# Optimization experiments

Measured on AMD Instinct MI355X. Metric: run time of the kernel, lower is better.

The kernel has to match this reference:

```python
import jax, jax.numpy as jnp
import numpy as np

B, T, D, HD = 4, 4096, 1024, 64

def setup_inputs() -> dict:
    key = jax.random.key(0)
    kx, kq, kk, kv = jax.random.split(key, 4)
    s = 1.0 / np.sqrt(D)
    return {
        "x": jax.random.normal(kx, (B, T, D), dtype=jnp.float32),
        "wq": jax.random.uniform(kq, (HD, D), jnp.float32, -s, s),
        "wk": jax.random.uniform(kk, (HD, D), jnp.float32, -s, s),
        "wv": jax.random.uniform(kv, (HD, D), jnp.float32, -s, s),
    }

def reference(x, wq, wk, wv):
    # Linear(D, headDim, bias=False): y = x @ W.T with W of shape [headDim, D]
    Q = jnp.einsum('btD,dD->btd', x, wq)
    K = jnp.einsum('bsD,dD->bsd', x, wk)
    V = jnp.einsum('bsD,dD->bsd', x, wv)
    head_dim = wq.shape[0]
    logits = jnp.einsum('btd,bsd->bts', Q, K) / jnp.sqrt(jnp.float32(head_dim))
    attn = jax.nn.softmax(logits, axis=-1)
    return jnp.einsum('bts,bsd->btd', attn, V)
```

## Files before the change

kernel.cpp:

```cpp
#include <hip/hip_runtime.h>
#include <math.h>

#define TLEN 4096
#define BD   1024
#define HDIM 64
#define NB   4

typedef __attribute__((ext_vector_type(8))) short bf16x8;
typedef __attribute__((ext_vector_type(4))) float f32x4;

typedef const __attribute__((address_space(1))) unsigned char* gp_t;
typedef __attribute__((address_space(3))) unsigned char* lp_t;

__device__ __forceinline__ void async_cp16(const void* g, void* l) {
    __builtin_amdgcn_global_load_lds((gp_t)g, (lp_t)l, 16, 0, 0);
}

__device__ __forceinline__ unsigned short f2bf(float f) {
    union { float f; unsigned u; } v; v.f = f;
    unsigned r = v.u + 0x7FFF + ((v.u >> 16) & 1);
    return (unsigned short)(r >> 16);
}

__device__ __forceinline__ bf16x8 cvt8(const float4 a, const float4 b) {
    bf16x8 r;
    r[0] = (short)f2bf(a.x); r[1] = (short)f2bf(a.y);
    r[2] = (short)f2bf(a.z); r[3] = (short)f2bf(a.w);
    r[4] = (short)f2bf(b.x); r[5] = (short)f2bf(b.y);
    r[6] = (short)f2bf(b.z); r[7] = (short)f2bf(b.w);
    return r;
}

__global__ __launch_bounds__(256) void wconv_kernel(
    const float* __restrict__ wq, const float* __restrict__ wk,
    const float* __restrict__ wv, unsigned short* __restrict__ wbf)
{
    const int r = blockIdx.x;
    const float* src = (r < 64) ? wq : (r < 128) ? wk : wv;
    const int rr = r & 63;
    const int c  = threadIdx.x * 4;
    float4 a = *(const float4*)&src[(size_t)rr * BD + c];
    uint2 o;
    o.x = (unsigned)f2bf(a.x) | ((unsigned)f2bf(a.y) << 16);
    o.y = (unsigned)f2bf(a.z) | ((unsigned)f2bf(a.w) << 16);
    *(uint2*)&wbf[(size_t)r * BD + c] = o;
}

__global__ __launch_bounds__(256, 2) void qkv_kernel(
    const float* __restrict__ x,
    const unsigned short* __restrict__ wbf,
    unsigned short* __restrict__ Qb,
    unsigned short* __restrict__ Kb,
    unsigned short* __restrict__ Vt)
{
    const int r0   = blockIdx.x * 32;
    const int tid  = threadIdx.x;
    const int lane = tid & 63;
    const int w    = tid >> 6;
    const int g    = lane >> 4;
    const int c    = lane & 15;

    __shared__ __align__(16) unsigned short wsh[2][192 * 64];
    __shared__ __align__(16) float          xf[2][32 * 64];
    __shared__ __align__(16) unsigned short vtr[64][40];

    f32x4 acc[3][2];
    #pragma unroll
    for (int t = 0; t < 3; ++t)
        #pragma unroll
        for (int rg = 0; rg < 2; ++rg) acc[t][rg] = (f32x4){0.f, 0.f, 0.f, 0.f};

    uint4 wreg[6];

    #define LOAD_W(k0s)                                                         \
        {                                                                       \
            _Pragma("unroll")                                                   \
            for (int ii = 0; ii < 6; ++ii) {                                    \
                const int L   = ii * 256 + tid;                                 \
                const int row = L >> 3;                                         \
                const int jl  = (L & 7) ^ (row & 7);                            \
                wreg[ii] = *(const uint4*)&wbf[(size_t)row * BD + (k0s) + jl * 8]; \
            }                                                                   \
        }
    #define WRITE_W(buf)                                                        \
        {                                                                       \
            _Pragma("unroll")                                                   \
            for (int ii = 0; ii < 6; ++ii) {                                    \
                const int L = ii * 256 + tid;                                   \
                *(uint4*)&wsh[buf][L * 8] = wreg[ii];                           \
            }                                                                   \
        }
    #define STAGE_X(buf, k0s)                                                   \
        {                                                                       \
            _Pragma("unroll")                                                   \
            for (int ii = 0; ii < 2; ++ii) {                                    \
                const int L   = ii * 256 + tid;                                 \
                const int row = L >> 4;                                         \
                const int gch = (L & 15) ^ (row & 15);                          \
                async_cp16(&x[(size_t)(r0 + row) * BD + (k0s) + gch * 4],       \
                           &xf[buf][L * 4]);                                    \
            }                                                                   \
        }

    LOAD_W(0)
    STAGE_X(0, 0)
    WRITE_W(0)

    for (int it = 0; it < 16; ++it) {
        const int cb = it & 1;
        __syncthreads();

        if (it < 15) {
            LOAD_W((it + 1) * 64)
            STAGE_X(cb ^ 1, (it + 1) * 64)
        }

        #pragma unroll
        for (int h = 0; h < 2; ++h) {
            const int oct = h * 4 + g;
            bf16x8 aX[2], bW[3];
            #pragma unroll
            for (int rg = 0; rg < 2; ++rg) {
                const int row = rg * 16 + c;
                const float4 a0 = *(const float4*)
                    &xf[cb][row * 64 + ((2 * oct) ^ c) * 4];
                const float4 a1 = *(const float4*)
                    &xf[cb][row * 64 + ((2 * oct + 1) ^ c) * 4];
                aX[rg] = cvt8(a0, a1);
            }
            const int slot = (oct ^ (c & 7)) * 8;
            #pragma unroll
            for (int t = 0; t < 3; ++t)
                bW[t] = *(const bf16x8*)&wsh[cb][((w * 3 + t) * 16 + c) * 64 + slot];
            #pragma unroll
            for (int t = 0; t < 3; ++t)
                #pragma unroll
                for (int rg = 0; rg < 2; ++rg)
                    acc[t][rg] = __builtin_amdgcn_mfma_f32_16x16x32_bf16(
                        aX[rg], bW[t], acc[t][rg], 0, 0, 0);
        }

        if (it < 15) WRITE_W(cb ^ 1)
    }

    const float qscale = 0.18033688f;
    const int   bb     = r0 / TLEN;
    const int   trow   = r0 % TLEN;
    #pragma unroll
    for (int t = 0; t < 3; ++t) {
        const int m = w * 3 + t;
        #pragma unroll
        for (int rg = 0; rg < 2; ++rg)
            #pragma unroll
            for (int i = 0; i < 4; ++i) {
                const int row = rg * 16 + g * 4 + i;
                if (m < 4)
                    Qb[(size_t)(r0 + row) * HDIM + m * 16 + c]
                        = f2bf(acc[t][rg][i] * qscale);
                else if (m < 8)
                    Kb[(size_t)(r0 + row) * HDIM + (m - 4) * 16 + c]
                        = f2bf(acc[t][rg][i]);
                else
                    vtr[(m - 8) * 16 + c][row] = f2bf(acc[t][rg][i]);
            }
    }
    __syncthreads();
    {
        const int d    = tid >> 2;
        const int part = tid & 3;
        uint4 v0 = *(const uint4*)&vtr[d][part * 8];
        unsigned short* dst = Vt + (size_t)bb * HDIM * TLEN + (size_t)d * TLEN
                            + trow + part * 8;
        *(uint4*)&dst[0] = v0;
    }
    #undef LOAD_W
    #undef WRITE_W
    #undef STAGE_X
}

template <int KEYS>
__global__ __launch_bounds__(256, 2) void attn_kernel(
    const unsigned short* __restrict__ Qb,
    const unsigned short* __restrict__ Kb,
    const unsigned short* __restrict__ Vt,
    float* __restrict__ O1, float* __restrict__ Ml, float* __restrict__ out)
{
    const int b     = blockIdx.y;
    const int q0    = blockIdx.x * 128;
    const int split = blockIdx.z;
    const int sbase = split * KEYS;

    const unsigned short* Qp = Qb + (size_t)b * TLEN * HDIM;
    const unsigned short* Kp = Kb + (size_t)b * TLEN * HDIM + (size_t)sbase * HDIM;
    const unsigned short* Vp = Vt + (size_t)b * HDIM * TLEN + sbase;

    const int tid  = threadIdx.x;
    const int lane = tid & 63;
    const int w    = tid >> 6;
    const int g    = lane >> 4;
    const int c    = lane & 15;

    __shared__ __align__(16) unsigned short ks[2][4096];
    __shared__ __align__(16) unsigned short vs[2][4096];
    __shared__ __align__(16) unsigned short pp[128][72];

    bf16x8 qB[2][2];
    #pragma unroll
    for (int h = 0; h < 2; ++h)
        #pragma unroll
        for (int kk = 0; kk < 2; ++kk)
            qB[h][kk] = *(const bf16x8*)
                &Qp[(size_t)(q0 + w * 32 + h * 16 + c) * HDIM + kk * 32 + g * 8];

    float lsum[2] = {0.f, 0.f};
    f32x4 oacc[2][4];
    #pragma unroll
    for (int h = 0; h < 2; ++h)
        #pragma unroll
        for (int t = 0; t < 4; ++t) oacc[h][t] = (f32x4){0.f, 0.f, 0.f, 0.f};

    const int nt = KEYS / 64;

    uint4 kreg[2], vreg[2];
    #define LOAD_KV(s0)                                                         \
        {                                                                       \
            _Pragma("unroll")                                                   \
            for (int ii = 0; ii < 2; ++ii) {                                    \
                const int L   = ii * 256 + tid;                                 \
                const int row = L >> 3;                                         \
                const int jl  = (L & 7) ^ (row & 7);                            \
                kreg[ii] = *(const uint4*)&Kp[(size_t)((s0) + row) * HDIM + jl * 8]; \
                vreg[ii] = *(const uint4*)&Vp[(size_t)row * TLEN + (s0) + jl * 8];   \
            }                                                                   \
        }
    #define WRITE_KV(buf)                                                       \
        {                                                                       \
            _Pragma("unroll")                                                   \
            for (int ii = 0; ii < 2; ++ii) {                                    \
                const int L = ii * 256 + tid;                                   \
                *(uint4*)&ks[buf][L * 8] = kreg[ii];                            \
                *(uint4*)&vs[buf][L * 8] = vreg[ii];                            \
            }                                                                   \
        }

    LOAD_KV(0)
    WRITE_KV(0)

    for (int it = 0; it < nt; ++it) {
        const int cb = it & 1;
        __syncthreads();

        if (it + 1 < nt) LOAD_KV((it + 1) * 64)

        f32x4 sacc[2][4];
        #pragma unroll
        for (int h = 0; h < 2; ++h)
            #pragma unroll
            for (int t = 0; t < 4; ++t) sacc[h][t] = (f32x4){0.f, 0.f, 0.f, 0.f};
        #pragma unroll
        for (int t = 0; t < 4; ++t) {
            const int r  = 16 * t + c;
            const int j0 = g ^ (r & 7);
            bf16x8 kA0 = *(const bf16x8*)&ks[cb][(r * 8 + j0) * 8];
            bf16x8 kA1 = *(const bf16x8*)&ks[cb][(r * 8 + (j0 ^ 4)) * 8];
            #pragma unroll
            for (int h = 0; h < 2; ++h) {
                sacc[h][t] = __builtin_amdgcn_mfma_f32_16x16x32_bf16(
                    kA0, qB[h][0], sacc[h][t], 0, 0, 0);
                sacc[h][t] = __builtin_amdgcn_mfma_f32_16x16x32_bf16(
                    kA1, qB[h][1], sacc[h][t], 0, 0, 0);
            }
        }

        if (it + 1 < nt) WRITE_KV(cb ^ 1)

        #pragma unroll
        for (int h = 0; h < 2; ++h) {
            const int qloc = w * 32 + h * 16 + c;
            #pragma unroll
            for (int t = 0; t < 4; ++t) {
                float p0 = __builtin_amdgcn_exp2f(sacc[h][t][0]);
                float p1 = __builtin_amdgcn_exp2f(sacc[h][t][1]);
                float p2 = __builtin_amdgcn_exp2f(sacc[h][t][2]);
                float p3 = __builtin_amdgcn_exp2f(sacc[h][t][3]);
                unsigned u0 = __float_as_uint(p0) & 0xffff0000u;
                unsigned u1 = __float_as_uint(p1) & 0xffff0000u;
                unsigned u2 = __float_as_uint(p2) & 0xffff0000u;
                unsigned u3 = __float_as_uint(p3) & 0xffff0000u;
                lsum[h] += (__uint_as_float(u0) + __uint_as_float(u1))
                         + (__uint_as_float(u2) + __uint_as_float(u3));
                uint2 pk;
                pk.x = (u0 >> 16) | u1;
                pk.y = (u2 >> 16) | u3;
                *(uint2*)&pp[qloc][16 * t + g * 4] = pk;
            }
        }

        bf16x8 pA[2][2];
        #pragma unroll
        for (int h = 0; h < 2; ++h) {
            pA[h][0] = *(const bf16x8*)&pp[w * 32 + h * 16 + c][g * 8];
            pA[h][1] = *(const bf16x8*)&pp[w * 32 + h * 16 + c][32 + g * 8];
        }
        #pragma unroll
        for (int t = 0; t < 4; ++t) {
            const int r  = 16 * t + c;
            const int j0 = g ^ (r & 7);
            bf16x8 vB0 = *(const bf16x8*)&vs[cb][(r * 8 + j0) * 8];
            bf16x8 vB1 = *(const bf16x8*)&vs[cb][(r * 8 + (j0 ^ 4)) * 8];
            #pragma unroll
            for (int h = 0; h < 2; ++h) {
                oacc[h][t] = __builtin_amdgcn_mfma_f32_16x16x32_bf16(
                    pA[h][0], vB0, oacc[h][t], 0, 0, 0);
                oacc[h][t] = __builtin_amdgcn_mfma_f32_16x16x32_bf16(
                    pA[h][1], vB1, oacc[h][t], 0, 0, 0);
            }
        }
    }
    #undef LOAD_KV
    #undef WRITE_KV

    #pragma unroll
    for (int h = 0; h < 2; ++h) {
        lsum[h] += __shfl_xor(lsum[h], 16);
        lsum[h] += __shfl_xor(lsum[h], 32);
    }

    #pragma unroll
    for (int h = 0; h < 2; ++h) {
        const size_t orow = (size_t)(b * TLEN + q0 + w * 32 + h * 16 + g * 4);
        if (KEYS == TLEN) {
            #pragma unroll
            for (int i = 0; i < 4; ++i) {
                const float inv = 1.0f / __shfl(lsum[h], g * 4 + i);
                #pragma unroll
                for (int t = 0; t < 4; ++t)
                    out[(orow + i) * HDIM + 16 * t + c] = oacc[h][t][i] * inv;
            }
        } else {
            float* Od = (split == 0)
                ? out : O1 + (size_t)(split - 1) * NB * TLEN * HDIM;
            #pragma unroll
            for (int i = 0; i < 4; ++i)
                #pragma unroll
                for (int t = 0; t < 4; ++t)
                    Od[(orow + i) * HDIM + 16 * t + c] = oacc[h][t][i];
            if (lane < 16)
                Ml[(size_t)(split * NB + b) * TLEN
                   + q0 + w * 32 + h * 16 + lane] = lsum[h];
        }
    }
}

__global__ __launch_bounds__(256) void merge_kernel(
    float* __restrict__ out, const float* __restrict__ O1,
    const float* __restrict__ Ml)
{
    const int idx  = blockIdx.x * 256 + threadIdx.x;
    const int row  = idx >> 4;
    const int col4 = (idx & 15) * 4;
    const int b    = row >> 12;
    const int t    = row & (TLEN - 1);
    float l = 0.f;
    #pragma unroll
    for (int s = 0; s < 4; ++s) l += Ml[(size_t)(s * NB + b) * TLEN + t];
    const float inv = 1.0f / l;
    float4 a = *(const float4*)&out[(size_t)row * HDIM + col4];
    #pragma unroll
    for (int s = 1; s < 4; ++s) {
        float4 p = *(const float4*)
            &O1[(size_t)(s - 1) * NB * TLEN * HDIM + (size_t)row * HDIM + col4];
        a.x += p.x; a.y += p.y; a.z += p.z; a.w += p.w;
    }
    a.x *= inv; a.y *= inv; a.z *= inv; a.w *= inv;
    *(float4*)&out[(size_t)row * HDIM + col4] = a;
}

extern "C" void kernel_launch(void* const* d_in, const int* in_sizes, int n_in,
                              void* d_out, int out_size, void* d_ws, size_t ws_size,
                              hipStream_t stream)
{
    (void)in_sizes; (void)n_in; (void)out_size;
    const float* x  = (const float*)d_in[0];
    const float* wq = (const float*)d_in[1];
    const float* wk = (const float*)d_in[2];
    const float* wv = (const float*)d_in[3];
    float* out = (float*)d_out;

    unsigned short* wbf = (unsigned short*)d_out;
    unsigned short* Qbf = (unsigned short*)d_ws;
    unsigned short* Kbf = Qbf + (size_t)NB * TLEN * HDIM;
    unsigned short* Vtb = Kbf + (size_t)NB * TLEN * HDIM;
    float* Ml = (float*)((char*)d_ws + (size_t)3 * NB * TLEN * HDIM * 2);
    float* O1 = Ml + (size_t)4 * NB * TLEN;
    const size_t ws_need = (size_t)3 * NB * TLEN * HDIM * 2
                         + (size_t)4 * NB * TLEN * 4
                         + (size_t)3 * NB * TLEN * HDIM * 4;
    const bool use_split = ws_size >= ws_need;

    wconv_kernel<<<dim3(192), 256, 0, stream>>>(wq, wk, wv, wbf);
    qkv_kernel<<<dim3(NB * TLEN / 32), 256, 0, stream>>>(x, wbf, Qbf, Kbf, Vtb);

    if (use_split) {
        attn_kernel<TLEN / 4><<<dim3(TLEN / 128, NB, 4), 256, 0, stream>>>(
            Qbf, Kbf, Vtb, O1, Ml, out);
        merge_kernel<<<dim3(NB * TLEN * 16 / 256), 256, 0, stream>>>(out, O1, Ml);
    } else {
        attn_kernel<TLEN><<<dim3(TLEN / 128, NB, 1), 256, 0, stream>>>(
            Qbf, Kbf, Vtb, O1, Ml, out);
    }
}
```

Measured before the change: 150.3 us.

## Switch attention to 32x32x16 MFMA with register-resident P via permlane32 swap

Rewrites the attention inner loop to use 32x32x16 bf16 MFMA tiles instead of 16x16x32. The softmax probabilities are converted with the hardware packed bf16 conversion and rearranged across lanes with permlane32_swap into the A-operand layout. This removes the LDS round trip through the pp buffer, cuts shared memory use and LDS traffic, and issues fewer, larger MFMAs. P rounding changes from truncation to round-to-nearest, and the output store pattern now follows the 32x32 accumulator layout.

```diff
diff --git a/kernel.cpp b/kernel.cpp
--- a/kernel.cpp
+++ b/kernel.cpp
@@ -8,6 +8,7 @@
 
 typedef __attribute__((ext_vector_type(8))) short bf16x8;
 typedef __attribute__((ext_vector_type(4))) float f32x4;
+typedef __attribute__((ext_vector_type(16))) float f32x16;
 
 typedef const __attribute__((address_space(1))) unsigned char* gp_t;
 typedef __attribute__((address_space(3))) unsigned char* lp_t;
@@ -28,6 +29,12 @@
     r[2] = (short)f2bf(a.z); r[3] = (short)f2bf(a.w);
     r[4] = (short)f2bf(b.x); r[5] = (short)f2bf(b.y);
     r[6] = (short)f2bf(b.z); r[7] = (short)f2bf(b.w);
+    return r;
+}
+
+__device__ __forceinline__ unsigned cvt_pk_bf16(float lo, float hi) {
+    unsigned r;
+    asm("v_cvt_pk_bf16_f32 %0, %1, %2" : "=v"(r) : "v"(lo), "v"(hi));
     return r;
 }
 
@@ -197,27 +204,25 @@
     const int tid  = threadIdx.x;
     const int lane = tid & 63;
     const int w    = tid >> 6;
-    const int g    = lane >> 4;
-    const int c    = lane & 15;
-
-    __shared__ __align__(16) unsigned short ks[2][4096];
-    __shared__ __align__(16) unsigned short vs[2][4096];
-    __shared__ __align__(16) unsigned short pp[128][72];
-
-    bf16x8 qB[2][2];
-    #pragma unroll
-    for (int h = 0; h < 2; ++h)
-        #pragma unroll
-        for (int kk = 0; kk < 2; ++kk)
-            qB[h][kk] = *(const bf16x8*)
-                &Qp[(size_t)(q0 + w * 32 + h * 16 + c) * HDIM + kk * 32 + g * 8];
-
-    float lsum[2] = {0.f, 0.f};
-    f32x4 oacc[2][4];
-    #pragma unroll
-    for (int h = 0; h < 2; ++h)
-        #pragma unroll
-        for (int t = 0; t < 4; ++t) oacc[h][t] = (f32x4){0.f, 0.f, 0.f, 0.f};
+    const int ql   = lane & 31;
+    const int hi   = lane >> 5;
+    const int ch   = lane & 7;
+
+    __shared__ __align__(16) unsigned short ksh[2][4096];
+    __shared__ __align__(16) unsigned short vsh[2][4096];
+
+    bf16x8 qB[4];
+    #pragma unroll
+    for (int s = 0; s < 4; ++s)
+        qB[s] = *(const bf16x8*)
+            &Qp[(size_t)(q0 + w * 32 + ql) * HDIM + s * 16 + hi * 8];
+
+    float  lsum = 0.f;
+    f32x16 oacc[2];
+    #pragma unroll
+    for (int dt = 0; dt < 2; ++dt)
+        #pragma unroll
+        for (int i = 0; i < 16; ++i) oacc[dt][i] = 0.f;
 
     const int nt = KEYS / 64;
 
@@ -238,8 +243,8 @@
             _Pragma("unroll")                                                   \
             for (int ii = 0; ii < 2; ++ii) {                                    \
                 const int L = ii * 256 + tid;                                   \
-                *(uint4*)&ks[buf][L * 8] = kreg[ii];                            \
-                *(uint4*)&vs[buf][L * 8] = vreg[ii];                            \
+                *(uint4*)&ksh[buf][L * 8] = kreg[ii];                           \
+                *(uint4*)&vsh[buf][L * 8] = vreg[ii];                           \
             }                                                                   \
         }
 
@@ -252,103 +257,85 @@
 
         if (it + 1 < nt) LOAD_KV((it + 1) * 64)
 
-        f32x4 sacc[2][4];
-        #pragma unroll
-        for (int h = 0; h < 2; ++h)
-            #pragma unroll
-            for (int t = 0; t < 4; ++t) sacc[h][t] = (f32x4){0.f, 0.f, 0.f, 0.f};
-        #pragma unroll
-        for (int t = 0; t < 4; ++t) {
-            const int r  = 16 * t + c;
-            const int j0 = g ^ (r & 7);
-            bf16x8 kA0 = *(const bf16x8*)&ks[cb][(r * 8 + j0) * 8];
-            bf16x8 kA1 = *(const bf16x8*)&ks[cb][(r * 8 + (j0 ^ 4)) * 8];
-            #pragma unroll
-            for (int h = 0; h < 2; ++h) {
-                sacc[h][t] = __builtin_amdgcn_mfma_f32_16x16x32_bf16(
-                    kA0, qB[h][0], sacc[h][t], 0, 0, 0);
-                sacc[h][t] = __builtin_amdgcn_mfma_f32_16x16x32_bf16(
-                    kA1, qB[h][1], sacc[h][t], 0, 0, 0);
-            }
-        }
+        f32x16 sacc[2];
+        #pragma unroll
+        for (int kt = 0; kt < 2; ++kt)
+            #pragma unroll
+            for (int i = 0; i < 16; ++i) sacc[kt][i] = 0.f;
+        #pragma unroll
+        for (int kt = 0; kt < 2; ++kt)
+            #pragma unroll
+            for (int s = 0; s < 4; ++s) {
+                const bf16x8 kA = *(const bf16x8*)
+                    &ksh[cb][(32 * kt + ql) * 64 + ((2 * s + hi) ^ ch) * 8];
+                sacc[kt] = __builtin_amdgcn_mfma_f32_32x32x16_bf16(
+                    kA, qB[s], sacc[kt], 0, 0, 0);
+            }
 
         if (it + 1 < nt) WRITE_KV(cb ^ 1)
 
-        #pragma unroll
-        for (int h = 0; h < 2; ++h) {
-            const int qloc = w * 32 + h * 16 + c;
-            #pragma unroll
-            for (int t = 0; t < 4; ++t) {
-                float p0 = __builtin_amdgcn_exp2f(sacc[h][t][0]);
-                float p1 = __builtin_amdgcn_exp2f(sacc[h][t][1]);
-                float p2 = __builtin_amdgcn_exp2f(sacc[h][t][2]);
-                float p3 = __builtin_amdgcn_exp2f(sacc[h][t][3]);
-                unsigned u0 = __float_as_uint(p0) & 0xffff0000u;
-                unsigned u1 = __float_as_uint(p1) & 0xffff0000u;
-                unsigned u2 = __float_as_uint(p2) & 0xffff0000u;
-                unsigned u3 = __float_as_uint(p3) & 0xffff0000u;
-                lsum[h] += (__uint_as_float(u0) + __uint_as_float(u1))
-                         + (__uint_as_float(u2) + __uint_as_float(u3));
-                uint2 pk;
-                pk.x = (u0 >> 16) | u1;
-                pk.y = (u2 >> 16) | u3;
-                *(uint2*)&pp[qloc][16 * t + g * 4] = pk;
-            }
-        }
-
-        bf16x8 pA[2][2];
-        #pragma unroll
-        for (int h = 0; h < 2; ++h) {
-            pA[h][0] = *(const bf16x8*)&pp[w * 32 + h * 16 + c][g * 8];
-            pA[h][1] = *(const bf16x8*)&pp[w * 32 + h * 16 + c][32 + g * 8];
-        }
-        #pragma unroll
-        for (int t = 0; t < 4; ++t) {
-            const int r  = 16 * t + c;
-            const int j0 = g ^ (r & 7);
-            bf16x8 vB0 = *(const bf16x8*)&vs[cb][(r * 8 + j0) * 8];
-            bf16x8 vB1 = *(const bf16x8*)&vs[cb][(r * 8 + (j0 ^ 4)) * 8];
-            #pragma unroll
-            for (int h = 0; h < 2; ++h) {
-                oacc[h][t] = __builtin_amdgcn_mfma_f32_16x16x32_bf16(
-                    pA[h][0], vB0, oacc[h][t], 0, 0, 0);
-                oacc[h][t] = __builtin_amdgcn_mfma_f32_16x16x32_bf16(
-                    pA[h][1], vB1, oacc[h][t], 0, 0, 0);
-            }
-        }
+        bf16x8 paf[4];
+        #pragma unroll
+        for (int kt = 0; kt < 2; ++kt) {
+            float p[16];
+            #pragma unroll
+            for (int i = 0; i < 16; ++i)
+                p[i] = __builtin_amdgcn_exp2f(sacc[kt][i]);
+            lsum += (((p[0] + p[1]) + (p[2] + p[3]))
+                   + ((p[4] + p[5]) + (p[6] + p[7])))
+                  + (((p[8] + p[9]) + (p[10] + p[11]))
+                   + ((p[12] + p[13]) + (p[14] + p[15])));
+            #pragma unroll
+            for (int bb = 0; bb < 2; ++bb) {
+                const unsigned X0 = cvt_pk_bf16(p[8 * bb + 0], p[8 * bb + 1]);
+                const unsigned X1 = cvt_pk_bf16(p[8 * bb + 2], p[8 * bb + 3]);
+                const unsigned Z0 = cvt_pk_bf16(p[8 * bb + 4], p[8 * bb + 5]);
+                const unsigned Z1 = cvt_pk_bf16(p[8 * bb + 6], p[8 * bb + 7]);
+                auto s02 = __builtin_amdgcn_permlane32_swap(X0, Z0, false, false);
+                auto s13 = __builtin_amdgcn_permlane32_swap(X1, Z1, false, false);
+                union { unsigned u[4]; bf16x8 v; } pu;
+                pu.u[0] = s02[0]; pu.u[1] = s13[0];
+                pu.u[2] = s02[1]; pu.u[3] = s13[1];
+                paf[kt * 2 + bb] = pu.v;
+            }
+        }
+
+        #pragma unroll
+        for (int dt = 0; dt < 2; ++dt)
+            #pragma unroll
+            for (int s = 0; s < 4; ++s) {
+                const bf16x8 vB = *(const bf16x8*)
+                    &vsh[cb][(32 * dt + ql) * 64 + ((2 * s + hi) ^ ch) * 8];
+                oacc[dt] = __builtin_amdgcn_mfma_f32_32x32x16_bf16(
+                    paf[s], vB, oacc[dt], 0, 0, 0);
+            }
     }
     #undef LOAD_KV
     #undef WRITE_KV
 
-    #pragma unroll
-    for (int h = 0; h < 2; ++h) {
-        lsum[h] += __shfl_xor(lsum[h], 16);
-        lsum[h] += __shfl_xor(lsum[h], 32);
-    }
-
-    #pragma unroll
-    for (int h = 0; h < 2; ++h) {
-        const size_t orow = (size_t)(b * TLEN + q0 + w * 32 + h * 16 + g * 4);
-        if (KEYS == TLEN) {
-            #pragma unroll
-            for (int i = 0; i < 4; ++i) {
-                const float inv = 1.0f / __shfl(lsum[h], g * 4 + i);
-                #pragma unroll
-                for (int t = 0; t < 4; ++t)
-                    out[(orow + i) * HDIM + 16 * t + c] = oacc[h][t][i] * inv;
-            }
-        } else {
-            float* Od = (split == 0)
-                ? out : O1 + (size_t)(split - 1) * NB * TLEN * HDIM;
-            #pragma unroll
-            for (int i = 0; i < 4; ++i)
-                #pragma unroll
-                for (int t = 0; t < 4; ++t)
-                    Od[(orow + i) * HDIM + 16 * t + c] = oacc[h][t][i];
-            if (lane < 16)
-                Ml[(size_t)(split * NB + b) * TLEN
-                   + q0 + w * 32 + h * 16 + lane] = lsum[h];
-        }
+    lsum += __shfl_xor(lsum, 32);
+
+    if (KEYS == TLEN) {
+        #pragma unroll
+        for (int r = 0; r < 16; ++r) {
+            const int   qr   = (r & 3) + 8 * (r >> 2) + 4 * hi;
+            const float inv  = 1.0f / __shfl(lsum, qr);
+            const size_t orow = (size_t)b * TLEN + q0 + w * 32 + qr;
+            out[orow * HDIM + ql]      = oacc[0][r] * inv;
+            out[orow * HDIM + 32 + ql] = oacc[1][r] * inv;
+        }
+    } else {
+        float* Od = (split == 0)
+            ? out : O1 + (size_t)(split - 1) * NB * TLEN * HDIM;
+        #pragma unroll
+        for (int r = 0; r < 16; ++r) {
+            const int   qr   = (r & 3) + 8 * (r >> 2) + 4 * hi;
+            const size_t orow = (size_t)b * TLEN + q0 + w * 32 + qr;
+            Od[orow * HDIM + ql]      = oacc[0][r];
+            Od[orow * HDIM + 32 + ql] = oacc[1][r];
+        }
+        if (lane < 32)
+            Ml[(size_t)(split * NB + b) * TLEN + q0 + w * 32 + lane] = lsum;
     }
 }
 
```

Result: faster. 144.7 us (-3.7%).
